# Optimization experiments

Measured on AMD Instinct MI355X. Metric: run time of the kernel, lower is better.

## Reference

```python
import jax, jax.numpy as jnp
import numpy as np

B, T, HID = 64, 512, 8192
C = 64            # num_channels (graph nodes)
NH = 4            # attention heads
HD = 16           # head_dim = graph_dim // num_heads
GD = 64           # graph_dim
IN_DIM = 128      # input_dim = channel_dim


def setup_inputs() -> dict:
    key = jax.random.key(0)
    ks = jax.random.split(key, 7)
    return {
        "H": jax.random.normal(ks[0], (B, T, HID), jnp.float32),
        "W_embed": jax.random.normal(ks[1], (GD, IN_DIM), jnp.float32) * 0.05,
        "b_embed": jax.random.normal(ks[2], (GD,), jnp.float32) * 0.05,
        "Wh_w": jax.random.normal(ks[3], (NH, HD, GD), jnp.float32) * 0.1,
        "a_w": jax.random.normal(ks[4], (NH, 2 * HD), jnp.float32) * 0.1,
        "Wr": jax.random.normal(ks[5], (IN_DIM, GD), jnp.float32) * 0.1,
        "br": jax.random.normal(ks[6], (IN_DIM,), jnp.float32) * 0.05,
    }


def reference(H, W_embed, b_embed, Wh_w, a_w, Wr, br):
    b, t, hid = H.shape
    ch = hid // C  # = IN_DIM
    # channel-wise temporal mean pooling -> graph node inputs [B, C, ch]
    node_inputs = H.reshape(b, t, C, ch).mean(axis=1)
    # node embedding [B, C, GD]
    nodes = jnp.einsum('bcf,gf->bcg', node_inputs, W_embed) + b_embed
    # per-head projection [B, NH, C, HD]
    Wh = jnp.einsum('bcg,hog->bhco', nodes, Wh_w)
    # split concat-score: cat([Wh_i, Wh_j]) @ a == (Wh@a1)_i + (Wh@a2)_j
    s1 = jnp.einsum('bhco,ho->bhc', Wh, a_w[:, :HD])
    s2 = jnp.einsum('bhco,ho->bhc', Wh, a_w[:, HD:])
    e = jax.nn.leaky_relu(s1[:, :, :, None] + s2[:, :, None, :], 0.2)  # [B,NH,C,C]
    attn = jax.nn.softmax(e, axis=-1)
    head_out = jax.nn.elu(jnp.einsum('bhij,bhjo->bhio', attn, Wh))  # [B,NH,C,HD]
    # concat heads along feature dim -> [B, C, GD]
    n_prime = head_out.transpose(0, 2, 1, 3).reshape(b, C, NH * HD)
    # readout on node-mean
    g = jax.nn.relu(jnp.einsum('bg,ig->bi', n_prime.mean(axis=1), Wr) + br)
    return g, attn
```

## Files before the change

kernel.cpp:

```cpp
#include <hip/hip_runtime.h>
#include <math.h>

#define NB 64
#define NT 512
#define HID 8192
#define NC 64
#define NH 4
#define HD 16
#define GD 64
#define IN_DIM 128
#define TSPLIT 4

typedef float f32x4 __attribute__((ext_vector_type(4)));

__global__ __launch_bounds__(256) void pool_kernel(const float* __restrict__ H,
                                                   float* __restrict__ part,
                                                   int ts_count) {
    const int b = blockIdx.y;
    const int ts = blockIdx.z;
    const int idx4 = blockIdx.x * 256 + threadIdx.x;
    const int rows = NT / ts_count;
    const f32x4* src = reinterpret_cast<const f32x4*>(H + (size_t)b * NT * HID) +
                       (size_t)(ts * rows) * (HID / 4) + idx4;
    f32x4 a0 = (f32x4)0.f;
    f32x4 a1 = (f32x4)0.f;
#pragma unroll 8
    for (int t = 0; t < rows; t += 2) {
        f32x4 v0 = __builtin_nontemporal_load(&src[(size_t)t * (HID / 4)]);
        f32x4 v1 = __builtin_nontemporal_load(&src[(size_t)(t + 1) * (HID / 4)]);
        a0 += v0;
        a1 += v1;
    }
    a0 += a1;
    reinterpret_cast<f32x4*>(part + ((size_t)ts * NB + b) * HID)[idx4] = a0;
}

__global__ __launch_bounds__(256) void embed_kernel(
    const float* __restrict__ part,
    const float* __restrict__ W_embed,
    const float* __restrict__ b_embed,
    const float* __restrict__ Wh_w,
    const float* __restrict__ a_w,
    float* __restrict__ Wh_out,
    float* __restrict__ s1_out,
    float* __restrict__ s2_out,
    int ts_count)
{
    __shared__ float sm_We[IN_DIM * GD];
    __shared__ float sm_Ww[GD * GD];
    __shared__ float sm_ni[16 * IN_DIM];
    __shared__ float sm_nodes[16 * GD];
    __shared__ float sm_Wh[16 * GD];

    const int tid = threadIdx.x;
    const int b = blockIdx.x;
    const int ct = blockIdx.y;

    for (int idx = tid; idx < IN_DIM * GD; idx += 256) {
        int g = idx >> 7, f = idx & 127;
        sm_We[f * GD + g] = W_embed[idx];
    }
    for (int idx = tid; idx < GD * GD; idx += 256) {
        int ho = idx >> 6, g = idx & 63;
        sm_Ww[g * GD + ho] = Wh_w[idx];
    }
    for (int idx4 = tid; idx4 < 16 * IN_DIM / 4; idx4 += 256) {
        f32x4 s = (f32x4)0.f;
        for (int ts = 0; ts < ts_count; ++ts) {
            f32x4 v = reinterpret_cast<const f32x4*>(
                &part[((size_t)ts * NB + b) * HID + ct * (16 * IN_DIM)])[idx4];
            s += v;
        }
        reinterpret_cast<f32x4*>(sm_ni)[idx4] = s * (1.0f / NT);
    }
    __syncthreads();

    {
        const int c = tid >> 4, g4 = (tid & 15) * 4;
        f32x4 acc = *reinterpret_cast<const f32x4*>(&b_embed[g4]);
#pragma unroll 8
        for (int f = 0; f < IN_DIM; ++f) {
            float n = sm_ni[c * IN_DIM + f];
            f32x4 w = *reinterpret_cast<const f32x4*>(&sm_We[f * GD + g4]);
            acc += n * w;
        }
        *reinterpret_cast<f32x4*>(&sm_nodes[c * GD + g4]) = acc;
    }
    __syncthreads();

    {
        const int c = tid >> 4, o4 = (tid & 15) * 4;
        f32x4 acc = (f32x4)0.f;
#pragma unroll 8
        for (int g = 0; g < GD; ++g) {
            float n = sm_nodes[c * GD + g];
            f32x4 w = *reinterpret_cast<const f32x4*>(&sm_Ww[g * GD + o4]);
            acc += n * w;
        }
        *reinterpret_cast<f32x4*>(&sm_Wh[c * GD + o4]) = acc;
        *reinterpret_cast<f32x4*>(
            &Wh_out[((size_t)b * NC + ct * 16 + c) * GD + o4]) = acc;
    }
    __syncthreads();

    if (tid < 64) {
        const int c = tid >> 2, h = tid & 3;
        float a1 = 0.f, a2 = 0.f;
#pragma unroll
        for (int o = 0; o < HD; ++o) {
            float w = sm_Wh[c * GD + h * HD + o];
            a1 += w * a_w[h * 2 * HD + o];
            a2 += w * a_w[h * 2 * HD + HD + o];
        }
        s1_out[((size_t)b * NH + h) * NC + ct * 16 + c] = a1;
        s2_out[((size_t)b * NH + h) * NC + ct * 16 + c] = a2;
    }
}

__global__ __launch_bounds__(256) void attn_kernel(
    const float* __restrict__ Wh_in,
    const float* __restrict__ s1_in,
    const float* __restrict__ s2_in,
    float* __restrict__ out_attn,
    float* __restrict__ mean_out)
{
    __shared__ float sm_Wh[NC * HD];
    __shared__ float sm_s1[NC], sm_s2[NC], sm_m[NC], sm_inv[NC];
    __shared__ float sm_ho[NC * HD];

    const int tid = threadIdx.x;
    const int b = blockIdx.x, h = blockIdx.y;

    {
        const int c = tid >> 2, p = tid & 3;
        *reinterpret_cast<f32x4*>(&sm_Wh[c * HD + p * 4]) =
            *reinterpret_cast<const f32x4*>(
                &Wh_in[((size_t)b * NC + c) * GD + h * HD + p * 4]);
    }
    if (tid < NC) sm_s1[tid] = s1_in[((size_t)b * NH + h) * NC + tid];
    else if (tid < 2 * NC) sm_s2[tid - NC] = s2_in[((size_t)b * NH + h) * NC + tid - NC];
    __syncthreads();

    if (tid < NC) {
        const float s1 = sm_s1[tid];
        float m = -1e30f;
        for (int j = 0; j < NC; ++j) {
            float x = s1 + sm_s2[j];
            float e = x > 0.f ? x : 0.2f * x;
            m = fmaxf(m, e);
        }
        float sum = 0.f;
        for (int j = 0; j < NC; ++j) {
            float x = s1 + sm_s2[j];
            float e = x > 0.f ? x : 0.2f * x;
            sum += __expf(e - m);
        }
        sm_m[tid] = m;
        sm_inv[tid] = 1.0f / sum;
    }
    __syncthreads();

    f32x4* attn_b = reinterpret_cast<f32x4*>(out_attn + ((size_t)b * NH + h) * NC * NC);
    for (int idx4 = tid; idx4 < NC * NC / 4; idx4 += 256) {
        const int i = idx4 >> 4, j = (idx4 & 15) * 4;
        const float s1 = sm_s1[i], m = sm_m[i], inv = sm_inv[i];
        f32x4 p;
        {
            float x = s1 + sm_s2[j + 0]; float e = x > 0.f ? x : 0.2f * x;
            p.x = __expf(e - m) * inv;
        }
        {
            float x = s1 + sm_s2[j + 1]; float e = x > 0.f ? x : 0.2f * x;
            p.y = __expf(e - m) * inv;
        }
        {
            float x = s1 + sm_s2[j + 2]; float e = x > 0.f ? x : 0.2f * x;
            p.z = __expf(e - m) * inv;
        }
        {
            float x = s1 + sm_s2[j + 3]; float e = x > 0.f ? x : 0.2f * x;
            p.w = __expf(e - m) * inv;
        }
        attn_b[idx4] = p;
    }

    {
        const int i = tid & 63, og = tid >> 6;
        const float s1 = sm_s1[i], m = sm_m[i], inv = sm_inv[i];
        float a0 = 0.f, a1 = 0.f, a2 = 0.f, a3 = 0.f;
        for (int j = 0; j < NC; ++j) {
            float x = s1 + sm_s2[j];
            float e = x > 0.f ? x : 0.2f * x;
            float p = __expf(e - m) * inv;
            const float* w = &sm_Wh[j * HD + og * 4];
            a0 += p * w[0]; a1 += p * w[1]; a2 += p * w[2]; a3 += p * w[3];
        }
        float* ho = &sm_ho[i * HD + og * 4];
        ho[0] = a0 > 0.f ? a0 : expm1f(a0);
        ho[1] = a1 > 0.f ? a1 : expm1f(a1);
        ho[2] = a2 > 0.f ? a2 : expm1f(a2);
        ho[3] = a3 > 0.f ? a3 : expm1f(a3);
    }
    __syncthreads();

    if (tid < HD) {
        float s = 0.f;
        for (int i = 0; i < NC; ++i) s += sm_ho[i * HD + tid];
        mean_out[(size_t)b * GD + h * HD + tid] = s * (1.0f / NC);
    }
}

__global__ __launch_bounds__(128) void readout_kernel(
    const float* __restrict__ mean_in,
    const float* __restrict__ Wr,
    const float* __restrict__ br,
    float* __restrict__ out_g)
{
    __shared__ float sm_mean[GD];
    __shared__ float sm_WrT[GD * (IN_DIM + 1)];

    const int tid = threadIdx.x;
    const int b = blockIdx.x;

    if (tid < GD) sm_mean[tid] = mean_in[(size_t)b * GD + tid];
    for (int idx = tid; idx < IN_DIM * GD; idx += 128) {
        int i = idx >> 6, g = idx & 63;
        sm_WrT[g * (IN_DIM + 1) + i] = Wr[idx];
    }
    __syncthreads();

    float acc = br[tid];
#pragma unroll 8
    for (int g = 0; g < GD; ++g)
        acc += sm_mean[g] * sm_WrT[g * (IN_DIM + 1) + tid];
    out_g[(size_t)b * IN_DIM + tid] = fmaxf(acc, 0.f);
}

extern "C" void kernel_launch(void* const* d_in, const int* in_sizes, int n_in,
                              void* d_out, int out_size, void* d_ws, size_t ws_size,
                              hipStream_t stream) {
    const float* H       = (const float*)d_in[0];
    const float* W_embed = (const float*)d_in[1];
    const float* b_embed = (const float*)d_in[2];
    const float* Wh_w    = (const float*)d_in[3];
    const float* a_w     = (const float*)d_in[4];
    const float* Wr      = (const float*)d_in[5];
    const float* br      = (const float*)d_in[6];
    float* out = (float*)d_out;
    float* out_attn = out + NB * IN_DIM;

    const size_t need4 = ((size_t)TSPLIT * NB * HID + NB * NC * GD +
                          2 * NB * NH * NC + NB * GD) * sizeof(float);
    const int ts = (ws_size >= need4) ? TSPLIT : 1;

    float* part   = (float*)d_ws;
    float* Wh_ws  = part + (size_t)ts * NB * HID;
    float* s1_ws  = Wh_ws + (size_t)NB * NC * GD;
    float* s2_ws  = s1_ws + (size_t)NB * NH * NC;
    float* mean_ws = s2_ws + (size_t)NB * NH * NC;

    dim3 g1(HID / 4 / 256, NB, ts);
    pool_kernel<<<g1, dim3(256), 0, stream>>>(H, part, ts);
    embed_kernel<<<dim3(NB, NC / 16), dim3(256), 0, stream>>>(
        part, W_embed, b_embed, Wh_w, a_w, Wh_ws, s1_ws, s2_ws, ts);
    attn_kernel<<<dim3(NB, NH), dim3(256), 0, stream>>>(
        Wh_ws, s1_ws, s2_ws, out_attn, mean_ws);
    readout_kernel<<<dim3(NB), dim3(128), 0, stream>>>(mean_ws, Wr, br, out);
}
```

Measured before the change: 193.9 us.

## Fuse readout into attention kernel via last-block atomic counter; cache attention probs

Removes the separate readout kernel launch: each attention block publishes its head mean with release stores and bumps a per-batch counter (zeroed in the pool kernel), and the last of the four head blocks performs the Wr readout. The attention probabilities are also written to a padded shared array so the head-output loop reuses them instead of recomputing exp. This trades a launch and redundant exp work for extra shared memory (about 50KB per block, possibly lowering occupancy) and atomic synchronisation.

```diff
diff --git a/kernel.cpp b/kernel.cpp
--- a/kernel.cpp
+++ b/kernel.cpp
@@ -15,9 +15,12 @@
 
 __global__ __launch_bounds__(256) void pool_kernel(const float* __restrict__ H,
                                                    float* __restrict__ part,
+                                                   unsigned* __restrict__ cnt,
                                                    int ts_count) {
     const int b = blockIdx.y;
     const int ts = blockIdx.z;
+    if (blockIdx.x == 0 && ts == 0 && threadIdx.x == 0) cnt[b] = 0u;
+
     const int idx4 = blockIdx.x * 256 + threadIdx.x;
     const int rows = NT / ts_count;
     const f32x4* src = reinterpret_cast<const f32x4*>(H + (size_t)b * NT * HID) +
@@ -121,12 +124,20 @@
     const float* __restrict__ Wh_in,
     const float* __restrict__ s1_in,
     const float* __restrict__ s2_in,
+    const float* __restrict__ Wr,
+    const float* __restrict__ br,
     float* __restrict__ out_attn,
-    float* __restrict__ mean_out)
+    float* __restrict__ out_g,
+    float* __restrict__ mean_ws,
+    unsigned* __restrict__ cnt)
 {
     __shared__ float sm_Wh[NC * HD];
     __shared__ float sm_s1[NC], sm_s2[NC], sm_m[NC], sm_inv[NC];
     __shared__ float sm_ho[NC * HD];
+    __shared__ float sm_p[NC * (NC + 1)];
+    __shared__ float sm_WrT[GD * (IN_DIM + 1)];
+    __shared__ float sm_mean[GD];
+    __shared__ unsigned sm_last;
 
     const int tid = threadIdx.x;
     const int b = blockIdx.x, h = blockIdx.y;
@@ -182,16 +193,17 @@
             p.w = __expf(e - m) * inv;
         }
         attn_b[idx4] = p;
-    }
+        float* pr = &sm_p[i * (NC + 1) + j];
+        pr[0] = p.x; pr[1] = p.y; pr[2] = p.z; pr[3] = p.w;
+    }
+    __syncthreads();
 
     {
         const int i = tid & 63, og = tid >> 6;
-        const float s1 = sm_s1[i], m = sm_m[i], inv = sm_inv[i];
         float a0 = 0.f, a1 = 0.f, a2 = 0.f, a3 = 0.f;
+        const float* prow = &sm_p[i * (NC + 1)];
         for (int j = 0; j < NC; ++j) {
-            float x = s1 + sm_s2[j];
-            float e = x > 0.f ? x : 0.2f * x;
-            float p = __expf(e - m) * inv;
+            float p = prow[j];
             const float* w = &sm_Wh[j * HD + og * 4];
             a0 += p * w[0]; a1 += p * w[1]; a2 += p * w[2]; a3 += p * w[3];
         }
@@ -206,34 +218,34 @@
     if (tid < HD) {
         float s = 0.f;
         for (int i = 0; i < NC; ++i) s += sm_ho[i * HD + tid];
-        mean_out[(size_t)b * GD + h * HD + tid] = s * (1.0f / NC);
-    }
-}
-
-__global__ __launch_bounds__(128) void readout_kernel(
-    const float* __restrict__ mean_in,
-    const float* __restrict__ Wr,
-    const float* __restrict__ br,
-    float* __restrict__ out_g)
-{
-    __shared__ float sm_mean[GD];
-    __shared__ float sm_WrT[GD * (IN_DIM + 1)];
-
-    const int tid = threadIdx.x;
-    const int b = blockIdx.x;
-
-    if (tid < GD) sm_mean[tid] = mean_in[(size_t)b * GD + tid];
-    for (int idx = tid; idx < IN_DIM * GD; idx += 128) {
-        int i = idx >> 6, g = idx & 63;
-        sm_WrT[g * (IN_DIM + 1) + i] = Wr[idx];
-    }
-    __syncthreads();
-
-    float acc = br[tid];
-#pragma unroll 8
-    for (int g = 0; g < GD; ++g)
-        acc += sm_mean[g] * sm_WrT[g * (IN_DIM + 1) + tid];
-    out_g[(size_t)b * IN_DIM + tid] = fmaxf(acc, 0.f);
+        __hip_atomic_store(&mean_ws[(size_t)b * GD + h * HD + tid], s * (1.0f / NC),
+                           __ATOMIC_RELEASE, __HIP_MEMORY_SCOPE_AGENT);
+    }
+    __syncthreads();
+
+    if (tid == 0) {
+        unsigned prev = __hip_atomic_fetch_add(&cnt[b], 1u, __ATOMIC_ACQ_REL,
+                                               __HIP_MEMORY_SCOPE_AGENT);
+        sm_last = (prev == NH - 1) ? 1u : 0u;
+    }
+    __syncthreads();
+    if (sm_last) {
+        if (tid < GD)
+            sm_mean[tid] = __hip_atomic_load(&mean_ws[(size_t)b * GD + tid],
+                                             __ATOMIC_ACQUIRE, __HIP_MEMORY_SCOPE_AGENT);
+        for (int idx = tid; idx < IN_DIM * GD; idx += 256) {
+            int i = idx >> 6, g = idx & 63;
+            sm_WrT[g * (IN_DIM + 1) + i] = Wr[idx];
+        }
+        __syncthreads();
+        if (tid < IN_DIM) {
+            float acc = br[tid];
+#pragma unroll 8
+            for (int g = 0; g < GD; ++g)
+                acc += sm_mean[g] * sm_WrT[g * (IN_DIM + 1) + tid];
+            out_g[(size_t)b * IN_DIM + tid] = fmaxf(acc, 0.f);
+        }
+    }
 }
 
 extern "C" void kernel_launch(void* const* d_in, const int* in_sizes, int n_in,
@@ -250,20 +262,20 @@
     float* out_attn = out + NB * IN_DIM;
 
     const size_t need4 = ((size_t)TSPLIT * NB * HID + NB * NC * GD +
-                          2 * NB * NH * NC + NB * GD) * sizeof(float);
+                          2 * NB * NH * NC + NB * GD + NB) * sizeof(float);
     const int ts = (ws_size >= need4) ? TSPLIT : 1;
 
-    float* part   = (float*)d_ws;
-    float* Wh_ws  = part + (size_t)ts * NB * HID;
-    float* s1_ws  = Wh_ws + (size_t)NB * NC * GD;
-    float* s2_ws  = s1_ws + (size_t)NB * NH * NC;
+    float* part    = (float*)d_ws;
+    float* Wh_ws   = part + (size_t)ts * NB * HID;
+    float* s1_ws   = Wh_ws + (size_t)NB * NC * GD;
+    float* s2_ws   = s1_ws + (size_t)NB * NH * NC;
     float* mean_ws = s2_ws + (size_t)NB * NH * NC;
+    unsigned* cnt  = (unsigned*)(mean_ws + (size_t)NB * GD);
 
     dim3 g1(HID / 4 / 256, NB, ts);
-    pool_kernel<<<g1, dim3(256), 0, stream>>>(H, part, ts);
+    pool_kernel<<<g1, dim3(256), 0, stream>>>(H, part, cnt, ts);
     embed_kernel<<<dim3(NB, NC / 16), dim3(256), 0, stream>>>(
         part, W_embed, b_embed, Wh_w, a_w, Wh_ws, s1_ws, s2_ws, ts);
     attn_kernel<<<dim3(NB, NH), dim3(256), 0, stream>>>(
-        Wh_ws, s1_ws, s2_ws, out_attn, mean_ws);
-    readout_kernel<<<dim3(NB), dim3(128), 0, stream>>>(mean_ws, Wr, br, out);
-}
+        Wh_ws, s1_ws, s2_ws, Wr, br, out_attn, out, mean_ws, cnt);
+}
```

Measured after the change: 198.3 us. +2.3%, slower.
